# Kernel tuning notes

Hardware: AMD Instinct MI355X
Metric: run time of the kernel (lower is better)

## Reference

```python
import jax, jax.numpy as jnp
import numpy as np

B, T, C, H = 2, 2048, 1024, 16
D = C // H  # head_dim = 64


def setup_inputs() -> dict:
    key = jax.random.key(0)
    k1, k2, k3 = jax.random.split(key, 3)
    scale = 0.02
    return {
        "x": jax.random.normal(k1, (B, T, C), dtype=jnp.float32),
        "w_qkv": jax.random.normal(k2, (C, 3 * C), dtype=jnp.float32) * scale,
        "b_qkv": jnp.zeros((3 * C,), dtype=jnp.float32),
        "w_out": jax.random.normal(k3, (C, C), dtype=jnp.float32) * scale,
        "b_out": jnp.zeros((C,), dtype=jnp.float32),
    }


def reference(x, w_qkv, b_qkv, w_out, b_out):
    b, t, c = x.shape
    qkv = x @ w_qkv + b_qkv                       # [b, t, 3c]
    q, k, v = jnp.split(qkv, 3, axis=-1)
    # [b, t, c] -> [b, h, t, d]
    q = q.reshape(b, t, H, D).transpose(0, 2, 1, 3)
    k = k.reshape(b, t, H, D).transpose(0, 2, 1, 3)
    v = v.reshape(b, t, H, D).transpose(0, 2, 1, 3)
    scores = jnp.einsum("bhqd,bhkd->bhqk", q, k) / jnp.sqrt(jnp.asarray(D, dtype=q.dtype))
    causal = jnp.tril(jnp.ones((t, t), dtype=bool))
    scores = jnp.where(causal, scores, jnp.finfo(scores.dtype).min)
    attn = jax.nn.softmax(scores, axis=-1)        # [b, h, q, k]
    out = jnp.einsum("bhqk,bhkd->bhqd", attn, v)  # [b, h, t, d]
    out = out.transpose(0, 2, 1, 3).reshape(b, t, c)
    return out @ w_out + b_out
```

## Files before the change

kernel.cpp:

```cpp
#include <hip/hip_runtime.h>

#define B_ 2
#define T_ 2048
#define C_ 1024
#define H_ 16
#define D_ 64
#define MLS (32 * 16 * 64)

using bf16x8 = __attribute__((ext_vector_type(8))) short;
using f32x4  = __attribute__((ext_vector_type(4))) float;

static __device__ __forceinline__ short f2bf(float f) {
  unsigned u = __builtin_bit_cast(unsigned, f);
  unsigned r = u + 0x7fffu + ((u >> 16) & 1u);
  return (short)(r >> 16);
}

#define GLD16(gp, lp) __builtin_amdgcn_global_load_lds( \
    (const __attribute__((address_space(1))) void*)(gp), \
    (__attribute__((address_space(3))) void*)(lp), 16, 0, 0)

__global__ __launch_bounds__(256) void prep(const float* __restrict__ x,
                                            const float* __restrict__ w_qkv,
                                            const float* __restrict__ w_out,
                                            short* __restrict__ xb,
                                            short* __restrict__ wqkvT,
                                            short* __restrict__ woutT) {
  const int blk = blockIdx.x;
  if (blk < 2048) {
    int base = blk * 2048 + threadIdx.x * 8;
    float4 a = *(const float4*)&x[base];
    float4 b = *(const float4*)&x[base + 4];
    short r[8];
    r[0] = f2bf(a.x); r[1] = f2bf(a.y); r[2] = f2bf(a.z); r[3] = f2bf(a.w);
    r[4] = f2bf(b.x); r[5] = f2bf(b.y); r[6] = f2bf(b.z); r[7] = f2bf(b.w);
    *(int4*)&xb[base] = *(int4*)r;
  } else {
    __shared__ float tile[32][33];
    const float* in; short* out; int R, N, tix, tiy;
    if (blk < 2048 + 3072) {
      int t = blk - 2048;
      in = w_qkv; out = wqkvT; R = 1024; N = 3072; tix = t % 96; tiy = t / 96;
    } else {
      int t = blk - 2048 - 3072;
      in = w_out; out = woutT; R = 1024; N = 1024; tix = t & 31; tiy = t >> 5;
    }
    const int bx = tix * 32, by = tiy * 32;
    const int tx = threadIdx.x & 31, ty = threadIdx.x >> 5;
    #pragma unroll
    for (int j = 0; j < 32; j += 8)
      tile[ty + j][tx] = in[(size_t)(by + ty + j) * N + bx + tx];
    __syncthreads();
    const int s = threadIdx.x;
    if (s < 128) {
      int row = s >> 2, seg = (s & 3) * 8;
      short r[8];
      #pragma unroll
      for (int j = 0; j < 8; ++j) r[j] = f2bf(tile[seg + j][row]);
      *(int4*)&out[(size_t)(bx + row) * R + by + seg] = *(int4*)r;
    }
  }
}

__global__ __launch_bounds__(256) void gemm_qkv(const short* __restrict__ A,
                                                const short* __restrict__ Bt,
                                                const float* __restrict__ bias,
                                                short* __restrict__ Qo,
                                                short* __restrict__ Ko,
                                                short* __restrict__ Vt) {
  __shared__ short smem[128 * 132];
  short* sA = smem;
  short* sB = smem + 128 * 64;
  const int tid = threadIdx.x;
  const int w = tid >> 6, lane = tid & 63;
  const int wm = w >> 1, wn = w & 1;
  const int g = lane >> 4, r16 = lane & 15;
  const int m0 = blockIdx.x * 128, n0 = blockIdx.y * 128;
  const int krow = lane >> 3, kslot = lane & 7;

  f32x4 acc[4][4] = {};

  for (int k0 = 0; k0 < 1024; k0 += 64) {
    __syncthreads();
    #pragma unroll
    for (int p = 0; p < 4; ++p) {
      int rbase = w * 32 + p * 8;
      int row = rbase + krow;
      GLD16(&A[(size_t)(m0 + row) * 1024 + k0 + ((kslot ^ (row & 7)) * 8)], &sA[rbase * 64]);
      GLD16(&Bt[(size_t)(n0 + row) * 1024 + k0 + ((kslot ^ (row & 7)) * 8)], &sB[rbase * 64]);
    }
    __syncthreads();
    bf16x8 af[4][2], bf[4][2];
    #pragma unroll
    for (int mi = 0; mi < 4; ++mi) {
      int row = wm * 64 + mi * 16 + r16;
      #pragma unroll
      for (int c = 0; c < 2; ++c)
        af[mi][c] = *(const bf16x8*)&sA[row * 64 + (((c * 4 + g) ^ (row & 7)) * 8)];
    }
    #pragma unroll
    for (int ni = 0; ni < 4; ++ni) {
      int row = wn * 64 + ni * 16 + r16;
      #pragma unroll
      for (int c = 0; c < 2; ++c)
        bf[ni][c] = *(const bf16x8*)&sB[row * 64 + (((c * 4 + g) ^ (row & 7)) * 8)];
    }
    __builtin_amdgcn_s_setprio(1);
    #pragma unroll
    for (int mi = 0; mi < 4; ++mi)
      #pragma unroll
      for (int ni = 0; ni < 4; ++ni) {
        acc[mi][ni] = __builtin_amdgcn_mfma_f32_16x16x32_bf16(af[mi][0], bf[ni][0], acc[mi][ni], 0, 0, 0);
        acc[mi][ni] = __builtin_amdgcn_mfma_f32_16x16x32_bf16(af[mi][1], bf[ni][1], acc[mi][ni], 0, 0, 0);
      }
    __builtin_amdgcn_s_setprio(0);
  }

  const int b2 = m0 >> 11, t0l = m0 & 2047;
  __syncthreads();

  if (n0 < 2048) {
    const int which = n0 >> 10;
    short* dst = (which == 0) ? Qo : Ko;
    const float sc = (which == 0) ? 0.18033688f : 1.0f;
    #pragma unroll
    for (int mi = 0; mi < 4; ++mi) {
      #pragma unroll
      for (int ni = 0; ni < 4; ++ni) {
        int nn = wn * 64 + ni * 16 + r16;
        float bv = bias[n0 + nn];
        #pragma unroll
        for (int rr = 0; rr < 4; ++rr) {
          int tm = wm * 64 + mi * 16 + g * 4 + rr;
          smem[tm * 132 + nn] = f2bf((acc[mi][ni][rr] + bv) * sc);
        }
      }
    }
    __syncthreads();
    const int h0 = (n0 & 1023) >> 6;
    const int c = lane & 15;
    const int head = h0 + (c >> 3);
    #pragma unroll
    for (int it = 0; it < 8; ++it) {
      int row = w * 32 + it * 4 + (lane >> 4);
      int4 v = *(const int4*)&smem[row * 132 + c * 8];
      *(int4*)&dst[(size_t)((b2 * H_ + head) * T_ + t0l + row) * 64 + (c & 7) * 8] = v;
    }
  } else {
    #pragma unroll
    for (int mi = 0; mi < 4; ++mi) {
      #pragma unroll
      for (int ni = 0; ni < 4; ++ni) {
        int nn = wn * 64 + ni * 16 + r16;
        float bv = bias[n0 + nn];
        #pragma unroll
        for (int rr = 0; rr < 4; ++rr) {
          int tm = wm * 64 + mi * 16 + g * 4 + rr;
          int tp = (tm & ~0x1C) | ((tm & 0xC) << 1) | ((tm & 0x10) >> 2);
          smem[nn * 132 + tp] = f2bf(acc[mi][ni][rr] + bv);
        }
      }
    }
    __syncthreads();
    const int head0 = b2 * H_ + ((n0 - 2048) >> 6);
    const int c = lane & 15;
    #pragma unroll
    for (int it = 0; it < 8; ++it) {
      int row = w * 32 + it * 4 + (lane >> 4);
      int d = row & 63, hh2 = row >> 6;
      int4 v = *(const int4*)&smem[row * 132 + c * 8];
      *(int4*)&Vt[((size_t)(head0 + hh2) * D_ + d) * T_ + t0l + c * 8] = v;
    }
  }
}

__global__ __launch_bounds__(256) void gemm_out(const short* __restrict__ A,
                                                const short* __restrict__ Bt,
                                                const float* __restrict__ bias,
                                                float* __restrict__ Out) {
  __shared__ short sA[128 * 64];
  __shared__ short sB[64 * 64];
  const int tid = threadIdx.x;
  const int w = tid >> 6, lane = tid & 63;
  const int wm = w >> 1, wn = w & 1;
  const int g = lane >> 4, r16 = lane & 15;
  const int m0 = blockIdx.x * 128, n0 = blockIdx.y * 64;
  const int krow = lane >> 3, kslot = lane & 7;

  f32x4 acc[4][2] = {};

  for (int k0 = 0; k0 < 1024; k0 += 64) {
    __syncthreads();
    #pragma unroll
    for (int p = 0; p < 4; ++p) {
      int rbase = w * 32 + p * 8;
      int row = rbase + krow;
      GLD16(&A[(size_t)(m0 + row) * 1024 + k0 + ((kslot ^ (row & 7)) * 8)], &sA[rbase * 64]);
    }
    #pragma unroll
    for (int p = 0; p < 2; ++p) {
      int rbase = w * 16 + p * 8;
      int row = rbase + krow;
      GLD16(&Bt[(size_t)(n0 + row) * 1024 + k0 + ((kslot ^ (row & 7)) * 8)], &sB[rbase * 64]);
    }
    __syncthreads();
    bf16x8 af[4][2], bf[2][2];
    #pragma unroll
    for (int mi = 0; mi < 4; ++mi) {
      int row = wm * 64 + mi * 16 + r16;
      #pragma unroll
      for (int c = 0; c < 2; ++c)
        af[mi][c] = *(const bf16x8*)&sA[row * 64 + (((c * 4 + g) ^ (row & 7)) * 8)];
    }
    #pragma unroll
    for (int ni = 0; ni < 2; ++ni) {
      int row = wn * 32 + ni * 16 + r16;
      #pragma unroll
      for (int c = 0; c < 2; ++c)
        bf[ni][c] = *(const bf16x8*)&sB[row * 64 + (((c * 4 + g) ^ (row & 7)) * 8)];
    }
    __builtin_amdgcn_s_setprio(1);
    #pragma unroll
    for (int mi = 0; mi < 4; ++mi)
      #pragma unroll
      for (int ni = 0; ni < 2; ++ni) {
        acc[mi][ni] = __builtin_amdgcn_mfma_f32_16x16x32_bf16(af[mi][0], bf[ni][0], acc[mi][ni], 0, 0, 0);
        acc[mi][ni] = __builtin_amdgcn_mfma_f32_16x16x32_bf16(af[mi][1], bf[ni][1], acc[mi][ni], 0, 0, 0);
      }
    __builtin_amdgcn_s_setprio(0);
  }

  #pragma unroll
  for (int mi = 0; mi < 4; ++mi) {
    #pragma unroll
    for (int ni = 0; ni < 2; ++ni) {
      int n = n0 + wn * 32 + ni * 16 + r16;
      float bv = bias[n];
      #pragma unroll
      for (int rr = 0; rr < 4; ++rr) {
        int m = m0 + wm * 64 + mi * 16 + g * 4 + rr;
        Out[(size_t)m * 1024 + n] = acc[mi][ni][rr] + bv;
      }
    }
  }
}

__global__ __launch_bounds__(256, 4) void attn_fwd(const short* __restrict__ Q,
                                                   const short* __restrict__ K,
                                                   const short* __restrict__ Vt,
                                                   short* __restrict__ O,
                                                   short* __restrict__ part,
                                                   float* __restrict__ ml) {
  __shared__ short sK[2][64 * 64];
  __shared__ short vT[2][64 * 64];

  const int tid = threadIdx.x;
  const int w = tid >> 6, lane = tid & 63;
  const int g = lane >> 4, r16 = lane & 15;
  const int bh = blockIdx.x;
  const int b = bh >> 4, hh = bh & 15;
  const int yy = blockIdx.y;
  const int k3 = yy / 3, r3 = yy - 3 * k3;
  const int split = (r3 != 2);
  const int qi = split ? (31 - k3) : (15 - k3);
  const int half = split ? r3 : 0;
  const int q0 = qi * 64;
  const int kt0 = (split && half) ? ((qi + 1) >> 1) : 0;
  const int kt1 = (split && !half) ? ((qi + 1) >> 1) : (qi + 1);

  const short* Qh = Q + (size_t)bh * T_ * D_;
  const short* Kh = K + (size_t)bh * T_ * D_;
  const short* Vh = Vt + (size_t)bh * D_ * T_;

  const int krw = lane >> 3;
  const int kslot = lane & 7;

  const int qrow_a = q0 + w * 16 + r16;
  bf16x8 qf[2];
  qf[0] = *(const bf16x8*)&Qh[(size_t)qrow_a * 64 + g * 8];
  qf[1] = *(const bf16x8*)&Qh[(size_t)qrow_a * 64 + 32 + g * 8];

  f32x4 o[4] = {};
  float m_ = -1e30f, l_ = 0.f;

  {
    const int k0 = kt0 * 64;
    #pragma unroll
    for (int p = 0; p < 2; ++p) {
      int row = w * 16 + p * 8 + krw;
      GLD16(&Kh[(size_t)(k0 + row) * 64 + ((kslot ^ (row & 7)) * 8)],
            &sK[0][(w * 16 + p * 8) * 64]);
      GLD16(&Vh[(size_t)row * T_ + k0 + ((kslot ^ (row & 7)) * 8)],
            &vT[0][(w * 16 + p * 8) * 64]);
    }
  }
  __syncthreads();

  for (int kt = kt0; kt < kt1; ++kt) {
    const int cur = (kt - kt0) & 1, nxt = cur ^ 1;
    const int k0 = kt * 64;
    const bool pf = (kt + 1 < kt1);

    if (pf) {
      const int k1 = k0 + 64;
      #pragma unroll
      for (int p = 0; p < 2; ++p) {
        int row = w * 16 + p * 8 + krw;
        GLD16(&Kh[(size_t)(k1 + row) * 64 + ((kslot ^ (row & 7)) * 8)],
              &sK[nxt][(w * 16 + p * 8) * 64]);
        GLD16(&Vh[(size_t)row * T_ + k1 + ((kslot ^ (row & 7)) * 8)],
              &vT[nxt][(w * 16 + p * 8) * 64]);
      }
    }

    f32x4 s[4] = {};
    __builtin_amdgcn_s_setprio(1);
    #pragma unroll
    for (int nt = 0; nt < 4; ++nt) {
      const int row = nt * 16 + r16;
      const int sw8 = r16 & 7;
      bf16x8 kf0 = *(const bf16x8*)&sK[cur][row * 64 + ((g ^ sw8) * 8)];
      bf16x8 kf1 = *(const bf16x8*)&sK[cur][row * 64 + (((4 + g) ^ sw8) * 8)];
      s[nt] = __builtin_amdgcn_mfma_f32_16x16x32_bf16(kf0, qf[0], s[nt], 0, 0, 0);
      s[nt] = __builtin_amdgcn_mfma_f32_16x16x32_bf16(kf1, qf[1], s[nt], 0, 0, 0);
    }
    __builtin_amdgcn_s_setprio(0);

    if (kt == qi) {
      const int qrow = w * 16 + r16;
      #pragma unroll
      for (int nt = 0; nt < 4; ++nt)
        #pragma unroll
        for (int rr = 0; rr < 4; ++rr)
          if (nt * 16 + 4 * g + rr > qrow) s[nt][rr] = -1e30f;
    }
    float pmax = s[0][0];
    #pragma unroll
    for (int nt = 0; nt < 4; ++nt)
      #pragma unroll
      for (int rr = 0; rr < 4; ++rr)
        pmax = fmaxf(pmax, s[nt][rr]);
    if (!__all(pmax - m_ <= 8.0f)) {
      float rmax = fmaxf(pmax, __shfl_xor(pmax, 16));
      rmax = fmaxf(rmax, __shfl_xor(rmax, 32));
      float mn = fmaxf(m_, rmax);
      float al = __builtin_amdgcn_exp2f(m_ - mn);
      m_ = mn;
      l_ *= al;
      float av[4];
      #pragma unroll
      for (int rr = 0; rr < 4; ++rr) av[rr] = __shfl(al, 4 * g + rr, 16);
      #pragma unroll
      for (int nt = 0; nt < 4; ++nt)
        #pragma unroll
        for (int rr = 0; rr < 4; ++rr) o[nt][rr] *= av[rr];
    }
    float rs = 0.f;
    #pragma unroll
    for (int nt = 0; nt < 4; ++nt)
      #pragma unroll
      for (int rr = 0; rr < 4; ++rr) {
        float p = __builtin_amdgcn_exp2f(s[nt][rr] - m_);
        s[nt][rr] = p;
        rs += p;
      }
    l_ += rs;
    int pk[8];
    #pragma unroll
    for (int nt = 0; nt < 4; ++nt)
      #pragma unroll
      for (int h = 0; h < 2; ++h)
        asm("v_cvt_pk_bf16_f32 %0, %1, %2"
            : "=v"(pk[nt * 2 + h])
            : "v"(s[nt][2 * h]), "v"(s[nt][2 * h + 1]));

    bf16x8 pa[2];
    {
      int4 t0; t0.x = pk[0]; t0.y = pk[1]; t0.z = pk[2]; t0.w = pk[3];
      int4 t1; t1.x = pk[4]; t1.y = pk[5]; t1.z = pk[6]; t1.w = pk[7];
      pa[0] = __builtin_bit_cast(bf16x8, t0);
      pa[1] = __builtin_bit_cast(bf16x8, t1);
    }
    __builtin_amdgcn_s_setprio(1);
    #pragma unroll
    for (int nt = 0; nt < 4; ++nt) {
      const int d = nt * 16 + r16;
      bf16x8 vb0 = *(const bf16x8*)&vT[cur][d * 64 + ((g ^ (d & 7)) * 8)];
      bf16x8 vb1 = *(const bf16x8*)&vT[cur][d * 64 + (((4 + g) ^ (d & 7)) * 8)];
      o[nt] = __builtin_amdgcn_mfma_f32_16x16x32_bf16(pa[0], vb0, o[nt], 0, 0, 0);
      o[nt] = __builtin_amdgcn_mfma_f32_16x16x32_bf16(pa[1], vb1, o[nt], 0, 0, 0);
    }
    __builtin_amdgcn_s_setprio(0);

    __syncthreads();
  }

  float lt = l_ + __shfl_xor(l_, 16);
  lt += __shfl_xor(lt, 32);
  float lv[4];
  #pragma unroll
  for (int rr = 0; rr < 4; ++rr) lv[rr] = __shfl(lt, 4 * g + rr, 16);

  if (!split || half == 0) {
    #pragma unroll
    for (int nt = 0; nt < 4; ++nt) {
      int d = nt * 16 + r16;
      #pragma unroll
      for (int rr = 0; rr < 4; ++rr) {
        int t = q0 + w * 16 + 4 * g + rr;
        O[(size_t)(b * T_ + t) * C_ + hh * 64 + d] = f2bf(o[nt][rr] / lv[rr]);
      }
    }
  } else {
    const int p = qi - 16;
    #pragma unroll
    for (int nt = 0; nt < 4; ++nt) {
      int d = nt * 16 + r16;
      #pragma unroll
      for (int rr = 0; rr < 4; ++rr) {
        int row = w * 16 + 4 * g + rr;
        part[((size_t)((bh * 16 + p) * 64 + row)) * 64 + d] = f2bf(o[nt][rr] / lv[rr]);
      }
    }
  }
  if (split && lane < 16) {
    const int p = qi - 16;
    int mi = (bh * 16 + p) * 64 + w * 16 + lane;
    ml[half * MLS + mi] = m_;
    ml[(2 + half) * MLS + mi] = lt;
  }
}

__global__ __launch_bounds__(256) void attn_combine(const short* __restrict__ part,
                                                    const float* __restrict__ ml,
                                                    short* __restrict__ O) {
  const int bh = blockIdx.x, p = blockIdx.y;
  const int qi = 16 + p;
  const int b = bh >> 4, hh = bh & 15;
  const int tid = threadIdx.x;
  const int row = tid >> 2;
  const int d0 = (tid & 3) * 16;
  const int mi = (bh * 16 + p) * 64 + row;
  float m1 = ml[mi],           m2 = ml[MLS + mi];
  float l1 = ml[2 * MLS + mi], l2 = ml[3 * MLS + mi];
  float ms = fmaxf(m1, m2);
  float w1 = l1 * __builtin_amdgcn_exp2f(m1 - ms);
  float w2 = l2 * __builtin_amdgcn_exp2f(m2 - ms);
  float inv = 1.0f / (w1 + w2);
  w1 *= inv; w2 *= inv;
  short* op = O + ((size_t)(b * T_ + qi * 64 + row) * C_) + hh * 64 + d0;
  const short* pp = part + ((size_t)((bh * 16 + p) * 64 + row)) * 64 + d0;
  #pragma unroll
  for (int v = 0; v < 2; ++v) {
    int4 a = *(const int4*)(op + v * 8);
    int4 c = *(const int4*)(pp + v * 8);
    const short* as = (const short*)&a;
    const short* cs = (const short*)&c;
    short r[8];
    #pragma unroll
    for (int j = 0; j < 8; ++j) {
      float o1 = __builtin_bit_cast(float, ((unsigned)(unsigned short)as[j]) << 16);
      float o2 = __builtin_bit_cast(float, ((unsigned)(unsigned short)cs[j]) << 16);
      r[j] = f2bf(w1 * o1 + w2 * o2);
    }
    *(int4*)(op + v * 8) = *(int4*)r;
  }
}

extern "C" void kernel_launch(void* const* d_in, const int* in_sizes, int n_in,
                              void* d_out, int out_size, void* d_ws, size_t ws_size,
                              hipStream_t stream) {
  const float* x     = (const float*)d_in[0];
  const float* w_qkv = (const float*)d_in[1];
  const float* b_qkv = (const float*)d_in[2];
  const float* w_out = (const float*)d_in[3];
  const float* b_out = (const float*)d_in[4];
  float* out = (float*)d_out;

  char* ws = (char*)d_ws;
  if (ws_size < (size_t)(40u << 20)) return;

  short* xb     = (short*)(ws);
  short* wqkvT  = (short*)(ws + ((size_t)8u << 20));
  short* woutT  = (short*)(ws + ((size_t)14u << 20));
  short* Qb     = (short*)(ws + ((size_t)16u << 20));
  short* Kb     = (short*)(ws + ((size_t)24u << 20));
  short* Vtb    = (short*)(ws + ((size_t)32u << 20));
  short* attn_o = xb;
  short* part   = wqkvT;
  float* ml     = (float*)(ws + ((size_t)12u << 20));

  prep<<<6144, 256, 0, stream>>>(x, w_qkv, w_out, xb, wqkvT, woutT);
  gemm_qkv<<<dim3(32, 24), 256, 0, stream>>>(xb, wqkvT, b_qkv, Qb, Kb, Vtb);
  attn_fwd<<<dim3(32, 48), 256, 0, stream>>>(Qb, Kb, Vtb, attn_o, part, ml);
  attn_combine<<<dim3(32, 16), 256, 0, stream>>>(part, ml, attn_o);
  gemm_out<<<dim3(32, 16), 256, 0, stream>>>(attn_o, woutT, b_out, out);
}
```

Measured before the change: 107.9 us.

## Enlarge attention query tile to 128 rows and rebalance split-KV scheduling

Each attention workgroup now handles 128 query rows, with each wave holding two 16-row query fragments. Each K/V tile loaded into LDS therefore feeds twice as many MFMAs, which cuts LDS traffic and per-tile overhead relative to compute. The split-KV partitioning is rebuilt around 128-row tiles: tiles 7..15 are split in two halves, giving 25 y-blocks instead of 48 and 9 combine blocks. The partial buffers move to a dedicated workspace region. The cost is more register pressure and fewer workgroups, which can lower occupancy, and coarser causal masking wastes some work on the diagonal tiles.

```diff
diff --git a/kernel.cpp b/kernel.cpp
--- a/kernel.cpp
+++ b/kernel.cpp
@@ -5,7 +5,7 @@
 #define C_ 1024
 #define H_ 16
 #define D_ 64
-#define MLS (32 * 16 * 64)
+#define MLS2 (32 * 9 * 128)
 
 using bf16x8 = __attribute__((ext_vector_type(8))) short;
 using f32x4  = __attribute__((ext_vector_type(4))) float;
@@ -260,13 +260,13 @@
   const int bh = blockIdx.x;
   const int b = bh >> 4, hh = bh & 15;
   const int yy = blockIdx.y;
-  const int k3 = yy / 3, r3 = yy - 3 * k3;
-  const int split = (r3 != 2);
-  const int qi = split ? (31 - k3) : (15 - k3);
-  const int half = split ? r3 : 0;
-  const int q0 = qi * 64;
-  const int kt0 = (split && half) ? ((qi + 1) >> 1) : 0;
-  const int kt1 = (split && !half) ? ((qi + 1) >> 1) : (qi + 1);
+  int j, half, split;
+  if (yy < 18) { split = 1; j = 15 - (yy >> 1); half = yy & 1; }
+  else         { split = 0; j = 24 - yy;        half = 0; }
+  const int q0 = j * 128;
+  const int nkt = 2 * j + 2;
+  const int kt0 = (split && half) ? (j + 1) : 0;
+  const int kt1 = (split && !half) ? (j + 1) : nkt;
 
   const short* Qh = Q + (size_t)bh * T_ * D_;
   const short* Kh = K + (size_t)bh * T_ * D_;
@@ -275,13 +275,16 @@
   const int krw = lane >> 3;
   const int kslot = lane & 7;
 
-  const int qrow_a = q0 + w * 16 + r16;
-  bf16x8 qf[2];
-  qf[0] = *(const bf16x8*)&Qh[(size_t)qrow_a * 64 + g * 8];
-  qf[1] = *(const bf16x8*)&Qh[(size_t)qrow_a * 64 + 32 + g * 8];
-
-  f32x4 o[4] = {};
-  float m_ = -1e30f, l_ = 0.f;
+  bf16x8 qf[2][2];
+  #pragma unroll
+  for (int u = 0; u < 2; ++u) {
+    const size_t qoff = (size_t)(q0 + w * 32 + u * 16 + r16) * 64;
+    qf[u][0] = *(const bf16x8*)&Qh[qoff + g * 8];
+    qf[u][1] = *(const bf16x8*)&Qh[qoff + 32 + g * 8];
+  }
+
+  f32x4 o[2][4] = {};
+  float m_[2] = {-1e30f, -1e30f}, l_[2] = {0.f, 0.f};
 
   {
     const int k0 = kt0 * 64;
@@ -313,7 +316,7 @@
       }
     }
 
-    f32x4 s[4] = {};
+    f32x4 s[2][4] = {};
     __builtin_amdgcn_s_setprio(1);
     #pragma unroll
     for (int nt = 0; nt < 4; ++nt) {
@@ -321,147 +324,157 @@
       const int sw8 = r16 & 7;
       bf16x8 kf0 = *(const bf16x8*)&sK[cur][row * 64 + ((g ^ sw8) * 8)];
       bf16x8 kf1 = *(const bf16x8*)&sK[cur][row * 64 + (((4 + g) ^ sw8) * 8)];
-      s[nt] = __builtin_amdgcn_mfma_f32_16x16x32_bf16(kf0, qf[0], s[nt], 0, 0, 0);
-      s[nt] = __builtin_amdgcn_mfma_f32_16x16x32_bf16(kf1, qf[1], s[nt], 0, 0, 0);
+      s[0][nt] = __builtin_amdgcn_mfma_f32_16x16x32_bf16(kf0, qf[0][0], s[0][nt], 0, 0, 0);
+      s[0][nt] = __builtin_amdgcn_mfma_f32_16x16x32_bf16(kf1, qf[0][1], s[0][nt], 0, 0, 0);
+      s[1][nt] = __builtin_amdgcn_mfma_f32_16x16x32_bf16(kf0, qf[1][0], s[1][nt], 0, 0, 0);
+      s[1][nt] = __builtin_amdgcn_mfma_f32_16x16x32_bf16(kf1, qf[1][1], s[1][nt], 0, 0, 0);
     }
     __builtin_amdgcn_s_setprio(0);
 
-    if (kt == qi) {
-      const int qrow = w * 16 + r16;
+    const bool msk = (kt >= 2 * j);
+    bf16x8 pa[2][2];
+    #pragma unroll
+    for (int u = 0; u < 2; ++u) {
+      if (msk) {
+        const int qrow = q0 + w * 32 + u * 16 + r16;
+        #pragma unroll
+        for (int nt = 0; nt < 4; ++nt)
+          #pragma unroll
+          for (int rr = 0; rr < 4; ++rr)
+            if (k0 + nt * 16 + 4 * g + rr > qrow) s[u][nt][rr] = -1e30f;
+      }
+      float pmax = s[u][0][0];
       #pragma unroll
       for (int nt = 0; nt < 4; ++nt)
         #pragma unroll
         for (int rr = 0; rr < 4; ++rr)
-          if (nt * 16 + 4 * g + rr > qrow) s[nt][rr] = -1e30f;
-    }
-    float pmax = s[0][0];
-    #pragma unroll
-    for (int nt = 0; nt < 4; ++nt)
-      #pragma unroll
-      for (int rr = 0; rr < 4; ++rr)
-        pmax = fmaxf(pmax, s[nt][rr]);
-    if (!__all(pmax - m_ <= 8.0f)) {
-      float rmax = fmaxf(pmax, __shfl_xor(pmax, 16));
-      rmax = fmaxf(rmax, __shfl_xor(rmax, 32));
-      float mn = fmaxf(m_, rmax);
-      float al = __builtin_amdgcn_exp2f(m_ - mn);
-      m_ = mn;
-      l_ *= al;
-      float av[4];
-      #pragma unroll
-      for (int rr = 0; rr < 4; ++rr) av[rr] = __shfl(al, 4 * g + rr, 16);
+          pmax = fmaxf(pmax, s[u][nt][rr]);
+      if (!__all(pmax - m_[u] <= 8.0f)) {
+        float rmax = fmaxf(pmax, __shfl_xor(pmax, 16));
+        rmax = fmaxf(rmax, __shfl_xor(rmax, 32));
+        float mn = fmaxf(m_[u], rmax);
+        float al = __builtin_amdgcn_exp2f(m_[u] - mn);
+        m_[u] = mn;
+        l_[u] *= al;
+        float av[4];
+        #pragma unroll
+        for (int rr = 0; rr < 4; ++rr) av[rr] = __shfl(al, 4 * g + rr, 16);
+        #pragma unroll
+        for (int nt = 0; nt < 4; ++nt)
+          #pragma unroll
+          for (int rr = 0; rr < 4; ++rr) o[u][nt][rr] *= av[rr];
+      }
+      float rs = 0.f;
       #pragma unroll
       for (int nt = 0; nt < 4; ++nt)
         #pragma unroll
-        for (int rr = 0; rr < 4; ++rr) o[nt][rr] *= av[rr];
-    }
-    float rs = 0.f;
-    #pragma unroll
-    for (int nt = 0; nt < 4; ++nt)
-      #pragma unroll
-      for (int rr = 0; rr < 4; ++rr) {
-        float p = __builtin_amdgcn_exp2f(s[nt][rr] - m_);
-        s[nt][rr] = p;
-        rs += p;
-      }
-    l_ += rs;
-    int pk[8];
-    #pragma unroll
-    for (int nt = 0; nt < 4; ++nt)
-      #pragma unroll
-      for (int h = 0; h < 2; ++h)
-        asm("v_cvt_pk_bf16_f32 %0, %1, %2"
-            : "=v"(pk[nt * 2 + h])
-            : "v"(s[nt][2 * h]), "v"(s[nt][2 * h + 1]));
-
-    bf16x8 pa[2];
-    {
+        for (int rr = 0; rr < 4; ++rr) {
+          float p = __builtin_amdgcn_exp2f(s[u][nt][rr] - m_[u]);
+          s[u][nt][rr] = p;
+          rs += p;
+        }
+      l_[u] += rs;
+      int pk[8];
+      #pragma unroll
+      for (int nt = 0; nt < 4; ++nt)
+        #pragma unroll
+        for (int h = 0; h < 2; ++h)
+          asm("v_cvt_pk_bf16_f32 %0, %1, %2"
+              : "=v"(pk[nt * 2 + h])
+              : "v"(s[u][nt][2 * h]), "v"(s[u][nt][2 * h + 1]));
       int4 t0; t0.x = pk[0]; t0.y = pk[1]; t0.z = pk[2]; t0.w = pk[3];
       int4 t1; t1.x = pk[4]; t1.y = pk[5]; t1.z = pk[6]; t1.w = pk[7];
-      pa[0] = __builtin_bit_cast(bf16x8, t0);
-      pa[1] = __builtin_bit_cast(bf16x8, t1);
-    }
+      pa[u][0] = __builtin_bit_cast(bf16x8, t0);
+      pa[u][1] = __builtin_bit_cast(bf16x8, t1);
+    }
+
     __builtin_amdgcn_s_setprio(1);
     #pragma unroll
     for (int nt = 0; nt < 4; ++nt) {
       const int d = nt * 16 + r16;
       bf16x8 vb0 = *(const bf16x8*)&vT[cur][d * 64 + ((g ^ (d & 7)) * 8)];
       bf16x8 vb1 = *(const bf16x8*)&vT[cur][d * 64 + (((4 + g) ^ (d & 7)) * 8)];
-      o[nt] = __builtin_amdgcn_mfma_f32_16x16x32_bf16(pa[0], vb0, o[nt], 0, 0, 0);
-      o[nt] = __builtin_amdgcn_mfma_f32_16x16x32_bf16(pa[1], vb1, o[nt], 0, 0, 0);
+      o[0][nt] = __builtin_amdgcn_mfma_f32_16x16x32_bf16(pa[0][0], vb0, o[0][nt], 0, 0, 0);
+      o[0][nt] = __builtin_amdgcn_mfma_f32_16x16x32_bf16(pa[0][1], vb1, o[0][nt], 0, 0, 0);
+      o[1][nt] = __builtin_amdgcn_mfma_f32_16x16x32_bf16(pa[1][0], vb0, o[1][nt], 0, 0, 0);
+      o[1][nt] = __builtin_amdgcn_mfma_f32_16x16x32_bf16(pa[1][1], vb1, o[1][nt], 0, 0, 0);
     }
     __builtin_amdgcn_s_setprio(0);
 
     __syncthreads();
   }
 
-  float lt = l_ + __shfl_xor(l_, 16);
-  lt += __shfl_xor(lt, 32);
-  float lv[4];
   #pragma unroll
-  for (int rr = 0; rr < 4; ++rr) lv[rr] = __shfl(lt, 4 * g + rr, 16);
-
-  if (!split || half == 0) {
-    #pragma unroll
-    for (int nt = 0; nt < 4; ++nt) {
-      int d = nt * 16 + r16;
-      #pragma unroll
-      for (int rr = 0; rr < 4; ++rr) {
-        int t = q0 + w * 16 + 4 * g + rr;
-        O[(size_t)(b * T_ + t) * C_ + hh * 64 + d] = f2bf(o[nt][rr] / lv[rr]);
-      }
-    }
-  } else {
-    const int p = qi - 16;
-    #pragma unroll
-    for (int nt = 0; nt < 4; ++nt) {
-      int d = nt * 16 + r16;
-      #pragma unroll
-      for (int rr = 0; rr < 4; ++rr) {
-        int row = w * 16 + 4 * g + rr;
-        part[((size_t)((bh * 16 + p) * 64 + row)) * 64 + d] = f2bf(o[nt][rr] / lv[rr]);
-      }
-    }
-  }
-  if (split && lane < 16) {
-    const int p = qi - 16;
-    int mi = (bh * 16 + p) * 64 + w * 16 + lane;
-    ml[half * MLS + mi] = m_;
-    ml[(2 + half) * MLS + mi] = lt;
+  for (int u = 0; u < 2; ++u) {
+    float lt = l_[u] + __shfl_xor(l_[u], 16);
+    lt += __shfl_xor(lt, 32);
+    float lv[4];
+    #pragma unroll
+    for (int rr = 0; rr < 4; ++rr) lv[rr] = __shfl(lt, 4 * g + rr, 16);
+
+    if (!split || half == 0) {
+      #pragma unroll
+      for (int nt = 0; nt < 4; ++nt) {
+        int d = nt * 16 + r16;
+        #pragma unroll
+        for (int rr = 0; rr < 4; ++rr) {
+          int t = q0 + w * 32 + u * 16 + 4 * g + rr;
+          O[(size_t)(b * T_ + t) * C_ + hh * 64 + d] = f2bf(o[u][nt][rr] / lv[rr]);
+        }
+      }
+    } else {
+      const int pj = j - 7;
+      #pragma unroll
+      for (int nt = 0; nt < 4; ++nt) {
+        int d = nt * 16 + r16;
+        #pragma unroll
+        for (int rr = 0; rr < 4; ++rr) {
+          int row = w * 32 + u * 16 + 4 * g + rr;
+          part[((size_t)((bh * 9 + pj) * 128 + row)) * 64 + d] = f2bf(o[u][nt][rr] / lv[rr]);
+        }
+      }
+    }
+    if (split && lane < 16) {
+      const int pj = j - 7;
+      int mi = (bh * 9 + pj) * 128 + w * 32 + u * 16 + lane;
+      ml[half * MLS2 + mi] = m_[u];
+      ml[(2 + half) * MLS2 + mi] = lt;
+    }
   }
 }
 
 __global__ __launch_bounds__(256) void attn_combine(const short* __restrict__ part,
                                                     const float* __restrict__ ml,
                                                     short* __restrict__ O) {
-  const int bh = blockIdx.x, p = blockIdx.y;
-  const int qi = 16 + p;
+  const int bh = blockIdx.x, pj = blockIdx.y;
+  const int j = pj + 7;
+  const int q0 = j * 128;
   const int b = bh >> 4, hh = bh & 15;
   const int tid = threadIdx.x;
-  const int row = tid >> 2;
-  const int d0 = (tid & 3) * 16;
-  const int mi = (bh * 16 + p) * 64 + row;
-  float m1 = ml[mi],           m2 = ml[MLS + mi];
-  float l1 = ml[2 * MLS + mi], l2 = ml[3 * MLS + mi];
+  const int row = tid >> 1;
+  const int d0 = (tid & 1) * 32;
+  const int mi = (bh * 9 + pj) * 128 + row;
+  float m1 = ml[mi],            m2 = ml[MLS2 + mi];
+  float l1 = ml[2 * MLS2 + mi], l2 = ml[3 * MLS2 + mi];
   float ms = fmaxf(m1, m2);
   float w1 = l1 * __builtin_amdgcn_exp2f(m1 - ms);
   float w2 = l2 * __builtin_amdgcn_exp2f(m2 - ms);
   float inv = 1.0f / (w1 + w2);
   w1 *= inv; w2 *= inv;
-  short* op = O + ((size_t)(b * T_ + qi * 64 + row) * C_) + hh * 64 + d0;
-  const short* pp = part + ((size_t)((bh * 16 + p) * 64 + row)) * 64 + d0;
+  short* op = O + ((size_t)(b * T_ + q0 + row) * C_) + hh * 64 + d0;
+  const short* pp = part + ((size_t)((bh * 9 + pj) * 128 + row)) * 64 + d0;
   #pragma unroll
-  for (int v = 0; v < 2; ++v) {
+  for (int v = 0; v < 4; ++v) {
     int4 a = *(const int4*)(op + v * 8);
     int4 c = *(const int4*)(pp + v * 8);
     const short* as = (const short*)&a;
     const short* cs = (const short*)&c;
     short r[8];
     #pragma unroll
-    for (int j = 0; j < 8; ++j) {
-      float o1 = __builtin_bit_cast(float, ((unsigned)(unsigned short)as[j]) << 16);
-      float o2 = __builtin_bit_cast(float, ((unsigned)(unsigned short)cs[j]) << 16);
-      r[j] = f2bf(w1 * o1 + w2 * o2);
+    for (int kk = 0; kk < 8; ++kk) {
+      float o1 = __builtin_bit_cast(float, ((unsigned)(unsigned short)as[kk]) << 16);
+      float o2 = __builtin_bit_cast(float, ((unsigned)(unsigned short)cs[kk]) << 16);
+      r[kk] = f2bf(w1 * o1 + w2 * o2);
     }
     *(int4*)(op + v * 8) = *(int4*)r;
   }
@@ -478,7 +491,7 @@
   float* out = (float*)d_out;
 
   char* ws = (char*)d_ws;
-  if (ws_size < (size_t)(40u << 20)) return;
+  if (ws_size < (size_t)(52u << 20)) return;
 
   short* xb     = (short*)(ws);
   short* wqkvT  = (short*)(ws + ((size_t)8u << 20));
@@ -487,12 +500,12 @@
   short* Kb     = (short*)(ws + ((size_t)24u << 20));
   short* Vtb    = (short*)(ws + ((size_t)32u << 20));
   short* attn_o = xb;
-  short* part   = wqkvT;
-  float* ml     = (float*)(ws + ((size_t)12u << 20));
+  short* part   = (short*)(ws + ((size_t)40u << 20));
+  float* ml     = (float*)(ws + ((size_t)50u << 20));
 
   prep<<<6144, 256, 0, stream>>>(x, w_qkv, w_out, xb, wqkvT, woutT);
   gemm_qkv<<<dim3(32, 24), 256, 0, stream>>>(xb, wqkvT, b_qkv, Qb, Kb, Vtb);
-  attn_fwd<<<dim3(32, 48), 256, 0, stream>>>(Qb, Kb, Vtb, attn_o, part, ml);
-  attn_combine<<<dim3(32, 16), 256, 0, stream>>>(part, ml, attn_o);
+  attn_fwd<<<dim3(32, 25), 256, 0, stream>>>(Qb, Kb, Vtb, attn_o, part, ml);
+  attn_combine<<<dim3(32, 9), 256, 0, stream>>>(part, ml, attn_o);
   gemm_out<<<dim3(32, 16), 256, 0, stream>>>(attn_o, woutT, b_out, out);
 }
```

Result: no change. 110.0 us (+1.9%).

## Fuse split-KV combine into attention via last-arriver atomic flag

Applied to the files above, without the earlier changes.

Removes the separate attn_combine kernel launch. Both halves of a split query tile now write their partial outputs and softmax stats to dedicated buffers and increment a per-tile atomic counter. The second block to arrive reads the other half through volatile loads, merges the two, and writes the final output. This saves one kernel launch and a round-trip through O, at the cost of extra workspace, fences, an atomic, and flag zeroing done in the prep kernel.

```diff
diff --git a/kernel.cpp b/kernel.cpp
--- a/kernel.cpp
+++ b/kernel.cpp
@@ -6,6 +6,7 @@
 #define H_ 16
 #define D_ 64
 #define MLS (32 * 16 * 64)
+#define PSZ ((size_t)32 * 16 * 64 * 64)
 
 using bf16x8 = __attribute__((ext_vector_type(8))) short;
 using f32x4  = __attribute__((ext_vector_type(4))) float;
@@ -25,8 +26,14 @@
                                             const float* __restrict__ w_out,
                                             short* __restrict__ xb,
                                             short* __restrict__ wqkvT,
-                                            short* __restrict__ woutT) {
+                                            short* __restrict__ woutT,
+                                            int* __restrict__ flags) {
   const int blk = blockIdx.x;
+  if (blk >= 6144) {
+    flags[threadIdx.x] = 0;
+    flags[256 + threadIdx.x] = 0;
+    return;
+  }
   if (blk < 2048) {
     int base = blk * 2048 + threadIdx.x * 8;
     float4 a = *(const float4*)&x[base];
@@ -250,9 +257,11 @@
                                                    const short* __restrict__ Vt,
                                                    short* __restrict__ O,
                                                    short* __restrict__ part,
-                                                   float* __restrict__ ml) {
+                                                   float* __restrict__ ml,
+                                                   int* __restrict__ flags) {
   __shared__ short sK[2][64 * 64];
   __shared__ short vT[2][64 * 64];
+  __shared__ int sflag;
 
   const int tid = threadIdx.x;
   const int w = tid >> 6, lane = tid & 63;
@@ -401,7 +410,7 @@
   #pragma unroll
   for (int rr = 0; rr < 4; ++rr) lv[rr] = __shfl(lt, 4 * g + rr, 16);
 
-  if (!split || half == 0) {
+  if (!split) {
     #pragma unroll
     for (int nt = 0; nt < 4; ++nt) {
       int d = nt * 16 + r16;
@@ -411,59 +420,64 @@
         O[(size_t)(b * T_ + t) * C_ + hh * 64 + d] = f2bf(o[nt][rr] / lv[rr]);
       }
     }
-  } else {
-    const int p = qi - 16;
-    #pragma unroll
-    for (int nt = 0; nt < 4; ++nt) {
-      int d = nt * 16 + r16;
-      #pragma unroll
-      for (int rr = 0; rr < 4; ++rr) {
-        int row = w * 16 + 4 * g + rr;
-        part[((size_t)((bh * 16 + p) * 64 + row)) * 64 + d] = f2bf(o[nt][rr] / lv[rr]);
-      }
-    }
-  }
-  if (split && lane < 16) {
-    const int p = qi - 16;
-    int mi = (bh * 16 + p) * 64 + w * 16 + lane;
+    return;
+  }
+
+  const int p = qi - 16;
+  const int base = (bh * 16 + p) * 64;
+  short* myp = part + half * PSZ;
+  #pragma unroll
+  for (int nt = 0; nt < 4; ++nt) {
+    int d = nt * 16 + r16;
+    #pragma unroll
+    for (int rr = 0; rr < 4; ++rr) {
+      int row = w * 16 + 4 * g + rr;
+      myp[((size_t)(base + row)) * 64 + d] = f2bf(o[nt][rr] / lv[rr]);
+    }
+  }
+  if (lane < 16) {
+    int mi = base + w * 16 + lane;
     ml[half * MLS + mi] = m_;
     ml[(2 + half) * MLS + mi] = lt;
   }
-}
-
-__global__ __launch_bounds__(256) void attn_combine(const short* __restrict__ part,
-                                                    const float* __restrict__ ml,
-                                                    short* __restrict__ O) {
-  const int bh = blockIdx.x, p = blockIdx.y;
-  const int qi = 16 + p;
-  const int b = bh >> 4, hh = bh & 15;
-  const int tid = threadIdx.x;
-  const int row = tid >> 2;
-  const int d0 = (tid & 3) * 16;
-  const int mi = (bh * 16 + p) * 64 + row;
-  float m1 = ml[mi],           m2 = ml[MLS + mi];
-  float l1 = ml[2 * MLS + mi], l2 = ml[3 * MLS + mi];
-  float ms = fmaxf(m1, m2);
-  float w1 = l1 * __builtin_amdgcn_exp2f(m1 - ms);
-  float w2 = l2 * __builtin_amdgcn_exp2f(m2 - ms);
-  float inv = 1.0f / (w1 + w2);
-  w1 *= inv; w2 *= inv;
-  short* op = O + ((size_t)(b * T_ + qi * 64 + row) * C_) + hh * 64 + d0;
-  const short* pp = part + ((size_t)((bh * 16 + p) * 64 + row)) * 64 + d0;
+  __threadfence();
+  __syncthreads();
+  if (tid == 0) sflag = atomicAdd(&flags[bh * 16 + p], 1);
+  __syncthreads();
+  if (sflag == 0) return;
+  __threadfence();
+
+  const int oh = 1 - half;
+  const volatile float* mlv = (const volatile float*)ml;
+  const volatile unsigned short* op2 =
+      (const volatile unsigned short*)(part + oh * PSZ);
+
+  float mmv[4], w1v[4], w2v[4];
   #pragma unroll
-  for (int v = 0; v < 2; ++v) {
-    int4 a = *(const int4*)(op + v * 8);
-    int4 c = *(const int4*)(pp + v * 8);
-    const short* as = (const short*)&a;
-    const short* cs = (const short*)&c;
-    short r[8];
-    #pragma unroll
-    for (int j = 0; j < 8; ++j) {
-      float o1 = __builtin_bit_cast(float, ((unsigned)(unsigned short)as[j]) << 16);
-      float o2 = __builtin_bit_cast(float, ((unsigned)(unsigned short)cs[j]) << 16);
-      r[j] = f2bf(w1 * o1 + w2 * o2);
-    }
-    *(int4*)(op + v * 8) = *(int4*)r;
+  for (int rr = 0; rr < 4; ++rr) {
+    int row = w * 16 + 4 * g + rr;
+    float m1 = __shfl(m_, 4 * g + rr, 16);
+    float l1 = lv[rr];
+    float m2 = mlv[oh * MLS + base + row];
+    float l2 = mlv[(2 + oh) * MLS + base + row];
+    float ms = fmaxf(m1, m2);
+    float w1 = l1 * __builtin_amdgcn_exp2f(m1 - ms);
+    float w2 = l2 * __builtin_amdgcn_exp2f(m2 - ms);
+    float inv = 1.0f / (w1 + w2);
+    mmv[rr] = ms; w1v[rr] = w1 * inv; w2v[rr] = w2 * inv;
+  }
+  #pragma unroll
+  for (int nt = 0; nt < 4; ++nt) {
+    int d = nt * 16 + r16;
+    #pragma unroll
+    for (int rr = 0; rr < 4; ++rr) {
+      int row = w * 16 + 4 * g + rr;
+      float mine = o[nt][rr] / lv[rr];
+      float other = __builtin_bit_cast(
+          float, ((unsigned)op2[((size_t)(base + row)) * 64 + d]) << 16);
+      int t = q0 + row;
+      O[(size_t)(b * T_ + t) * C_ + hh * 64 + d] = f2bf(w1v[rr] * mine + w2v[rr] * other);
+    }
   }
 }
 
@@ -478,7 +492,7 @@
   float* out = (float*)d_out;
 
   char* ws = (char*)d_ws;
-  if (ws_size < (size_t)(40u << 20)) return;
+  if (ws_size < (size_t)(52u << 20)) return;
 
   short* xb     = (short*)(ws);
   short* wqkvT  = (short*)(ws + ((size_t)8u << 20));
@@ -487,12 +501,12 @@
   short* Kb     = (short*)(ws + ((size_t)24u << 20));
   short* Vtb    = (short*)(ws + ((size_t)32u << 20));
   short* attn_o = xb;
-  short* part   = wqkvT;
-  float* ml     = (float*)(ws + ((size_t)12u << 20));
-
-  prep<<<6144, 256, 0, stream>>>(x, w_qkv, w_out, xb, wqkvT, woutT);
+  short* part   = (short*)(ws + ((size_t)40u << 20));
+  float* ml     = (float*)(ws + ((size_t)48u << 20));
+  int*   flags  = (int*)(ws + ((size_t)49u << 20));
+
+  prep<<<6145, 256, 0, stream>>>(x, w_qkv, w_out, xb, wqkvT, woutT, flags);
   gemm_qkv<<<dim3(32, 24), 256, 0, stream>>>(xb, wqkvT, b_qkv, Qb, Kb, Vtb);
-  attn_fwd<<<dim3(32, 48), 256, 0, stream>>>(Qb, Kb, Vtb, attn_o, part, ml);
-  attn_combine<<<dim3(32, 16), 256, 0, stream>>>(part, ml, attn_o);
+  attn_fwd<<<dim3(32, 48), 256, 0, stream>>>(Qb, Kb, Vtb, attn_o, part, ml, flags);
   gemm_out<<<dim3(32, 16), 256, 0, stream>>>(attn_o, woutT, b_out, out);
 }
```

Measured after the change: 293.6 us. 172% more time.
